# Optimization experiments

Measured on AMD Instinct MI355X. Metric: run time of the kernel, lower is better.

Reference implementation:

```python
import jax, jax.numpy as jnp
import numpy as np

N, F, E = 100000, 128, 600000
EPS = 1e-5

def setup_inputs() -> dict:
    key = jax.random.key(0)
    ks = jax.random.split(key, 12)
    d = {
        'feature': jax.random.normal(ks[0], (N, F), jnp.float32),
        'edge_index': jax.random.randint(ks[1], (2, E), 0, N, jnp.int64 if jax.config.jax_enable_x64 else jnp.int32).astype(jnp.int32),
        'edge_weight': jax.random.uniform(ks[2], (E,), jnp.float32),
        'Ws': jax.random.normal(ks[3], (F, F), jnp.float32) * (2.0 / F) ** 0.5,
        'bs': jnp.zeros((F,), jnp.float32),
        'Wi': jax.random.normal(ks[4], (F, F), jnp.float32) * (2.0 / F) ** 0.5,
        'bi': jnp.zeros((F,), jnp.float32),
        'Wr': jax.random.normal(ks[5], (F, F), jnp.float32) * (2.0 / F) ** 0.5,
        'br': jnp.zeros((F,), jnp.float32),
        'gamma': jnp.ones((F,), jnp.float32),
        'beta': jnp.zeros((F,), jnp.float32),
        'WtoI': jax.random.normal(ks[6], (2 * F, F), jnp.float32) * (1.0 / (2 * F)) ** 0.5,
        'btoI': jnp.zeros((F,), jnp.float32),
        'WtoR': jax.random.normal(ks[7], (F, F), jnp.float32) * (1.0 / F) ** 0.5,
        'btoR': jnp.zeros((F,), jnp.float32),
        'Wout': jax.random.normal(ks[8], (3 * F, 3), jnp.float32) * (2.0 / (3 * F)) ** 0.5,
        'bout': jnp.zeros((3,), jnp.float32),
    }
    return d

def _bn(x, gamma, beta):
    # BatchNorm1d in training mode: batch mean, biased variance
    m = x.mean(axis=0)
    v = x.var(axis=0)
    return gamma * (x - m) * jax.lax.rsqrt(v + EPS) + beta

def reference(feature, edge_index, edge_weight, Ws, bs, Wi, bi, Wr, br,
              gamma, beta, WtoI, btoI, WtoR, btoR, Wout, bout):
    n = feature.shape[0]
    s = jax.nn.relu(_bn(feature @ Ws + bs + feature, gamma, beta))
    i = jax.nn.relu(_bn(feature @ Wi + bi + feature, gamma, beta))
    r = jax.nn.relu(_bn(feature @ Wr + br + feature, gamma, beta))
    # message passing: gather i at source nodes, weight, scatter-add to dest
    src, dst = edge_index[0], edge_index[1]
    msg = i[src] * edge_weight[:, None]                      # [E, F]
    neighbor_i = jax.ops.segment_sum(msg, dst, num_segments=n)  # [N, F]
    toI = jnp.concatenate([s, neighbor_i], axis=1) @ WtoI + btoI
    toR = i @ WtoR + btoR
    s1 = s - toI
    i1 = i + toI - toR
    r1 = toR + r
    logits = jnp.concatenate([s1, i1, r1], axis=-1) @ Wout + bout  # [N, 3]
    return jax.nn.softmax(logits, axis=-1)
```

## Files before the change

kernel.cpp:

```cpp
#include <hip/hip_runtime.h>
#include <math.h>

#define NFEAT 128
#define EPSBN 1e-5f
#define LDA 136
#define NREP 8
#define G1GRID 1536

typedef __attribute__((ext_vector_type(8))) short short8;
typedef __attribute__((ext_vector_type(4))) float f32x4;

__device__ __forceinline__ unsigned short f2bf(float x) {
  union { float f; unsigned u; } v; v.f = x;
  unsigned r = v.u + 0x7FFF + ((v.u >> 16) & 1);
  return (unsigned short)(r >> 16);
}
__device__ __forceinline__ float bf2f(unsigned short h) {
  union { unsigned u; float f; } v; v.u = (unsigned)h << 16;
  return v.f;
}

__global__ __launch_bounds__(256) void kp_params(
    const float* __restrict__ Ws, const float* __restrict__ Wi,
    const float* __restrict__ Wr,
    const float* __restrict__ WtoI, const float* __restrict__ btoI,
    const float* __restrict__ WtoR, const float* __restrict__ btoR,
    const float* __restrict__ Wout, const float* __restrict__ bout,
    short* __restrict__ Whi,
    float* __restrict__ MT, float* __restrict__ cb)
{
  const int tid = threadIdx.x;
  if (blockIdx.x < 24) {
    int t = blockIdx.x * 256 + tid;
    int m   = t >> 11;
    int rem = t & 2047;
    int kf  = rem >> 9;
    int kg  = (rem >> 7) & 3;
    int c   = rem & 127;
    const float* W = (m == 0) ? Ws : ((m == 1) ? Wi : Wr);
    short hb[8];
#pragma unroll
    for (int j = 0; j < 8; j++) {
      int k = kf * 32 + kg * 8 + j;
      float w = W[(size_t)k * NFEAT + c] + (k == c ? 1.0f : 0.0f);
      hb[j] = (short)f2bf(w);
    }
    int base = ((m * 16 + kf * 4 + kg) << 10) + (c << 3);
    *(short8*)&Whi[base] = *(short8*)hb;
    return;
  }

  int t = (blockIdx.x - 24) * 256 + tid;
  int cl = t / 512;
  int idx = t - cl * 512;
  int part = idx >> 7, k = idx & 127;
  float val;
  if (part == 0) {
    float s = Wout[k * 3 + cl];
    for (int f = 0; f < 128; f++)
      s = fmaf(WtoI[k * 128 + f],
               Wout[(128 + f) * 3 + cl] - Wout[f * 3 + cl], s);
    val = s;
  } else if (part == 1) {
    float s = Wout[(128 + k) * 3 + cl];
    for (int f = 0; f < 128; f++)
      s = fmaf(WtoR[k * 128 + f],
               Wout[(256 + f) * 3 + cl] - Wout[(128 + f) * 3 + cl], s);
    val = s;
  } else if (part == 2) {
    val = Wout[(256 + k) * 3 + cl];
  } else {
    float s = 0.f;
    for (int f = 0; f < 128; f++)
      s = fmaf(WtoI[(128 + k) * 128 + f],
               Wout[(128 + f) * 3 + cl] - Wout[f * 3 + cl], s);
    val = s;
  }
  MT[cl * 512 + idx] = val;

  if (blockIdx.x == 24 && tid < 3) {
    float s = bout[tid];
    for (int f = 0; f < 128; f++) {
      s = fmaf(btoI[f], Wout[(128 + f) * 3 + tid] - Wout[f * 3 + tid], s);
      s = fmaf(btoR[f], Wout[(256 + f) * 3 + tid] - Wout[(128 + f) * 3 + tid], s);
    }
    cb[tid] = s;
  }
}

__global__ __launch_bounds__(256) void k1a_store(
    const float* __restrict__ feat,
    const short* __restrict__ Whi,
    const float* __restrict__ bs, const float* __restrict__ bi,
    const float* __restrict__ br,
    float* __restrict__ stats,
    unsigned short* __restrict__ Pb,
    int N, int ntiles)
{
  __shared__ short Ah[32 * LDA];

  const int tid  = threadIdx.x;
  const int lane = tid & 63;
  const int wv   = tid >> 6;
  const int l15  = lane & 15;
  const int kg   = lane >> 4;
  const int krow = kg * 8;
  const int sr   = tid >> 3;
  const int so   = tid & 7;

  const int col0 = wv * 32 + l15;
  const int col1 = wv * 32 + 16 + l15;

  float bias0[3], bias1[3];
  {
    const float* Bm[3] = {bs, bi, br};
#pragma unroll
    for (int m = 0; m < 3; m++) { bias0[m] = Bm[m][col0]; bias1[m] = Bm[m][col1]; }
  }
  float ssum0[3] = {0.f, 0.f, 0.f}, ssq0[3] = {0.f, 0.f, 0.f};
  float ssum1[3] = {0.f, 0.f, 0.f}, ssq1[3] = {0.f, 0.f, 0.f};
  const size_t nf = (size_t)N * NFEAT;

  for (int tile = blockIdx.x; tile < ntiles; tile += gridDim.x) {
    const int row0 = tile * 32;
    {
      int gr = row0 + sr; if (gr >= N) gr = N - 1;
      const float4* s4 = (const float4*)(feat + (size_t)gr * NFEAT + so * 16);
      short hbuf[16];
#pragma unroll
      for (int q = 0; q < 4; q++) {
        float4 f = s4[q];
        float xs[4] = {f.x, f.y, f.z, f.w};
#pragma unroll
        for (int cc = 0; cc < 4; cc++) hbuf[q * 4 + cc] = (short)f2bf(xs[cc]);
      }
      *(short8*)&Ah[sr * LDA + so * 16]     = *(short8*)(hbuf);
      *(short8*)&Ah[sr * LDA + so * 16 + 8] = *(short8*)(hbuf + 8);
    }
    asm volatile("s_waitcnt lgkmcnt(0)" ::: "memory");
    __builtin_amdgcn_s_barrier();

#pragma unroll
    for (int m = 0; m < 3; m++) {
      f32x4 a00 = {0.f,0.f,0.f,0.f}, a01 = {0.f,0.f,0.f,0.f};
      f32x4 a10 = {0.f,0.f,0.f,0.f}, a11 = {0.f,0.f,0.f,0.f};
#pragma unroll
      for (int kf = 0; kf < 4; kf++) {
        int fb0 = ((m * 16 + kf * 4 + kg) << 10) + (col0 << 3);
        int fb1 = ((m * 16 + kf * 4 + kg) << 10) + (col1 << 3);
        short8 b0 = *(const short8*)&Whi[fb0];
        short8 b1 = *(const short8*)&Whi[fb1];
        short8 ar0 = *(const short8*)&Ah[(l15) * LDA + kf * 32 + krow];
        short8 ar1 = *(const short8*)&Ah[(16 + l15) * LDA + kf * 32 + krow];
        a00 = __builtin_amdgcn_mfma_f32_16x16x32_bf16(ar0, b0, a00, 0, 0, 0);
        a01 = __builtin_amdgcn_mfma_f32_16x16x32_bf16(ar1, b0, a01, 0, 0, 0);
        a10 = __builtin_amdgcn_mfma_f32_16x16x32_bf16(ar0, b1, a10, 0, 0, 0);
        a11 = __builtin_amdgcn_mfma_f32_16x16x32_bf16(ar1, b1, a11, 0, 0, 0);
      }
#pragma unroll
      for (int g = 0; g < 4; g++) {
        int gr0 = row0 + kg * 4 + g;
        int gr1 = row0 + 16 + kg * 4 + g;
        if (gr0 < N) {
          float v = a00[g] + bias0[m];
          ssum0[m] += v; ssq0[m] += v * v;
          Pb[(size_t)m * nf + (size_t)gr0 * NFEAT + col0] = f2bf(v);
          float w = a10[g] + bias1[m];
          ssum1[m] += w; ssq1[m] += w * w;
          Pb[(size_t)m * nf + (size_t)gr0 * NFEAT + col1] = f2bf(w);
        }
        if (gr1 < N) {
          float v = a01[g] + bias0[m];
          ssum0[m] += v; ssq0[m] += v * v;
          Pb[(size_t)m * nf + (size_t)gr1 * NFEAT + col0] = f2bf(v);
          float w = a11[g] + bias1[m];
          ssum1[m] += w; ssq1[m] += w * w;
          Pb[(size_t)m * nf + (size_t)gr1 * NFEAT + col1] = f2bf(w);
        }
      }
    }
    asm volatile("s_waitcnt lgkmcnt(0)" ::: "memory");
    __builtin_amdgcn_s_barrier();
  }

#pragma unroll
  for (int m = 0; m < 3; m++) {
    float s0 = ssum0[m], q0 = ssq0[m], s1 = ssum1[m], q1 = ssq1[m];
    s0 += __shfl_xor(s0, 16); s0 += __shfl_xor(s0, 32);
    q0 += __shfl_xor(q0, 16); q0 += __shfl_xor(q0, 32);
    s1 += __shfl_xor(s1, 16); s1 += __shfl_xor(s1, 32);
    q1 += __shfl_xor(q1, 16); q1 += __shfl_xor(q1, 32);
    if (kg == 0) {
      unsafeAtomicAdd(&stats[m * 256 + col0], s0);
      unsafeAtomicAdd(&stats[m * 256 + 128 + col0], q0);
      unsafeAtomicAdd(&stats[m * 256 + col1], s1);
      unsafeAtomicAdd(&stats[m * 256 + 128 + col1], q1);
    }
  }
}

__global__ __launch_bounds__(256) void k1g_post(
    const unsigned short* __restrict__ Pb,
    const float* __restrict__ stats,
    const float* __restrict__ gamma, const float* __restrict__ beta,
    const float* __restrict__ MT,
    float* __restrict__ slogA, float* __restrict__ qv,
    float* __restrict__ logit3R, int N, int N4, int nrt, float invN)
{
  __shared__ float4 A4s[384];
  __shared__ float4 B4s[384];
  const int tid = threadIdx.x;
  for (int i = tid; i < 384; i += 256) {
    int m = i >> 7, c = i & 127;
    float mu = stats[m * 256 + c] * invN;
    float var = stats[m * 256 + 128 + c] * invN - mu * mu;
    float a = gamma[c] * rsqrtf(var + EPSBN);
    float kv = beta[c] - mu * a;
    int idx = m * 128 + (c & 7) * 16 + (c >> 3);
    A4s[idx] = make_float4(MT[0 * 512 + m * 128 + c],
                           MT[1 * 512 + m * 128 + c],
                           MT[2 * 512 + m * 128 + c], a);
    if (m == 1)
      B4s[idx] = make_float4(MT[0 * 512 + 384 + c],
                             MT[1 * 512 + 384 + c],
                             MT[2 * 512 + 384 + c], kv);
    else
      B4s[idx] = make_float4(0.f, 0.f, 0.f, kv);
  }
  __syncthreads();

  const int l15 = tid & 15;
  const int rg  = tid >> 4;
  const size_t nf = (size_t)N * NFEAT;

  for (int it = blockIdx.x; it < nrt; it += gridDim.x) {
    if (tid < 128) {
      int rep = tid >> 4;
      int zr = it * 16 + (tid & 15);
      if (zr < N)
        *(float4*)&logit3R[(size_t)rep * N4 + (size_t)zr * 4] =
            make_float4(0.f, 0.f, 0.f, 0.f);
    }

    int row = it * 16 + rg;
    if (row >= N) continue;

    float s0 = 0.f, s1 = 0.f, s2 = 0.f;
    float q0 = 0.f, q1 = 0.f, q2 = 0.f;
#pragma unroll
    for (int m = 0; m < 3; m++) {
      const uint4* p4 =
          (const uint4*)(Pb + (size_t)m * nf + (size_t)row * NFEAT + l15 * 8);
      uint4 u = p4[0];
      unsigned dw[4] = {u.x, u.y, u.z, u.w};
#pragma unroll
      for (int d = 0; d < 4; d++) {
        {
          float4 ab = A4s[m * 128 + (2 * d) * 16 + l15];
          float4 bq = B4s[m * 128 + (2 * d) * 16 + l15];
          float P = bf2f((unsigned short)(dw[d] & 0xffffu));
          float v = fmaxf(fmaf(ab.w, P, bq.w), 0.f);
          s0 = fmaf(v, ab.x, s0); s1 = fmaf(v, ab.y, s1); s2 = fmaf(v, ab.z, s2);
          q0 = fmaf(v, bq.x, q0); q1 = fmaf(v, bq.y, q1); q2 = fmaf(v, bq.z, q2);
        }
        {
          float4 ab = A4s[m * 128 + (2 * d + 1) * 16 + l15];
          float4 bq = B4s[m * 128 + (2 * d + 1) * 16 + l15];
          float P = bf2f((unsigned short)(dw[d] >> 16));
          float v = fmaxf(fmaf(ab.w, P, bq.w), 0.f);
          s0 = fmaf(v, ab.x, s0); s1 = fmaf(v, ab.y, s1); s2 = fmaf(v, ab.z, s2);
          q0 = fmaf(v, bq.x, q0); q1 = fmaf(v, bq.y, q1); q2 = fmaf(v, bq.z, q2);
        }
      }
    }
#pragma unroll
    for (int off = 1; off < 16; off <<= 1) {
      s0 += __shfl_xor(s0, off); s1 += __shfl_xor(s1, off);
      s2 += __shfl_xor(s2, off);
      q0 += __shfl_xor(q0, off); q1 += __shfl_xor(q1, off);
      q2 += __shfl_xor(q2, off);
    }
    if (l15 == 0) {
      *(float4*)&slogA[(size_t)row * 4] = make_float4(s0, s1, s2, 0.f);
      *(float4*)&qv[(size_t)row * 4]    = make_float4(q0, q1, q2, 0.f);
    }
  }
}

__global__ __launch_bounds__(256) void k_edge(
    const int* __restrict__ eidx, const float* __restrict__ ew,
    const float* __restrict__ q, float* __restrict__ logit3R,
    int E, int N4)
{
  const int wid  = (blockIdx.x * 256 + threadIdx.x) >> 6;
  const int lane = threadIdx.x & 63;
  const int el   = lane / 3;
  const int comp = lane - el * 3;
  if (el >= 21) return;
  const int e = wid * 21 + el;
  if (e >= E) return;

  int src = eidx[e];
  int dst = eidx[E + e];
  float w = ew[e];
  float qvv = q[(size_t)src * 4 + comp];
  int rep = wid & (NREP - 1);
  unsafeAtomicAdd(&logit3R[(size_t)rep * N4 + (size_t)dst * 4 + comp], qvv * w);
}

__global__ __launch_bounds__(256) void k4_final(
    const float* __restrict__ slogA, const float* __restrict__ logit3R,
    const float* __restrict__ cb,
    float* __restrict__ out, int N, int N4)
{
  int r = blockIdx.x * 256 + threadIdx.x;
  if (r >= N) return;
  float4 S = *(const float4*)&slogA[(size_t)r * 4];
  float l0 = S.x + cb[0], l1 = S.y + cb[1], l2 = S.z + cb[2];
#pragma unroll
  for (int rep = 0; rep < NREP; rep++) {
    float4 L = *(const float4*)&logit3R[(size_t)rep * N4 + (size_t)r * 4];
    l0 += L.x; l1 += L.y; l2 += L.z;
  }
  float mx = fmaxf(l0, fmaxf(l1, l2));
  float e0 = expf(l0 - mx), e1 = expf(l1 - mx), e2 = expf(l2 - mx);
  float inv = 1.f / (e0 + e1 + e2);
  out[(size_t)r * 3 + 0] = e0 * inv;
  out[(size_t)r * 3 + 1] = e1 * inv;
  out[(size_t)r * 3 + 2] = e2 * inv;
}

extern "C" void kernel_launch(void* const* d_in, const int* in_sizes, int n_in,
                              void* d_out, int out_size, void* d_ws, size_t ws_size,
                              hipStream_t stream)
{
  const float* feat  = (const float*)d_in[0];
  const int*   eidx  = (const int*)  d_in[1];
  const float* ew    = (const float*)d_in[2];
  const float* Ws    = (const float*)d_in[3];
  const float* bs    = (const float*)d_in[4];
  const float* Wi    = (const float*)d_in[5];
  const float* bi    = (const float*)d_in[6];
  const float* Wr    = (const float*)d_in[7];
  const float* br    = (const float*)d_in[8];
  const float* gamma = (const float*)d_in[9];
  const float* beta  = (const float*)d_in[10];
  const float* WtoI  = (const float*)d_in[11];
  const float* btoI  = (const float*)d_in[12];
  const float* WtoR  = (const float*)d_in[13];
  const float* btoR  = (const float*)d_in[14];
  const float* Wout  = (const float*)d_in[15];
  const float* bout  = (const float*)d_in[16];

  const int N = in_sizes[0] / NFEAT;
  const int E = in_sizes[2];
  const int N4 = 4 * N;
  const float invN = 1.0f / (float)N;
  float* out = (float*)d_out;

  float* logit3R = (float*)d_ws;
  float* slogA   = logit3R + (size_t)NREP * N4;
  float* qv      = slogA + 4 * (size_t)N;
  float* stats   = qv + 4 * (size_t)N;
  float* MT      = stats + 768;
  float* cb      = MT + 1536;
  short* Whi     = (short*)(cb + 4);
  unsigned short* Pb = (unsigned short*)(Whi + 49152);

  hipMemsetAsync(stats, 0, 768 * sizeof(float), stream);

  const int nt32 = (N + 31) / 32;
  const int nrt  = (N + 15) / 16;

  kp_params<<<30, 256, 0, stream>>>(Ws, Wi, Wr, WtoI, btoI, WtoR, btoR,
                                    Wout, bout, Whi, MT, cb);
  k1a_store<<<G1GRID, 256, 0, stream>>>(feat, Whi, bs, bi, br, stats, Pb,
                                        N, nt32);
  k1g_post<<<2048, 256, 0, stream>>>(Pb, stats, gamma, beta, MT,
                                     slogA, qv, logit3R, N, N4, nrt, invN);
  const int nwaves = (E + 20) / 21;
  k_edge<<<(nwaves + 3) / 4, 256, 0, stream>>>(eidx, ew, qv, logit3R, E, N4);
  k4_final<<<(N + 255) / 256, 256, 0, stream>>>(slogA, logit3R, cb, out, N, N4);
}
```

Baseline: 143.1 us.

## Replace BN-stat atomics with per-block partials and dedicated reduction kernel

Each k1a_store block now writes its per-column sum and sum-of-squares into a transposed partials buffer instead of issuing global float atomics into a shared stats array. A new k_redbn kernel reduces the partials per column, computes the BatchNorm scale and shift together with the MT coefficients once, and stores them as float4 tables. k1g_post then just loads these precomputed tables instead of having every block recompute them, and the memset is dropped. The aim is to remove atomic contention and the repeated per-block BN setup, at the cost of an extra kernel launch and roughly 4.7 MB of partials traffic.

Result: faster. 120.8 us (median of 2 runs) (-15.6%).

```diff
diff --git a/kernel.cpp b/kernel.cpp
--- a/kernel.cpp
+++ b/kernel.cpp
@@ -93,7 +93,7 @@
     const short* __restrict__ Whi,
     const float* __restrict__ bs, const float* __restrict__ bi,
     const float* __restrict__ br,
-    float* __restrict__ stats,
+    float* __restrict__ SpartT,
     unsigned short* __restrict__ Pb,
     int N, int ntiles)
 {
@@ -191,42 +191,70 @@
     s1 += __shfl_xor(s1, 16); s1 += __shfl_xor(s1, 32);
     q1 += __shfl_xor(q1, 16); q1 += __shfl_xor(q1, 32);
     if (kg == 0) {
-      unsafeAtomicAdd(&stats[m * 256 + col0], s0);
-      unsafeAtomicAdd(&stats[m * 256 + 128 + col0], q0);
-      unsafeAtomicAdd(&stats[m * 256 + col1], s1);
-      unsafeAtomicAdd(&stats[m * 256 + 128 + col1], q1);
-    }
+      SpartT[(size_t)(m * 256 + col0) * G1GRID + blockIdx.x]       = s0;
+      SpartT[(size_t)(m * 256 + 128 + col0) * G1GRID + blockIdx.x] = q0;
+      SpartT[(size_t)(m * 256 + col1) * G1GRID + blockIdx.x]       = s1;
+      SpartT[(size_t)(m * 256 + 128 + col1) * G1GRID + blockIdx.x] = q1;
+    }
+  }
+}
+
+__global__ __launch_bounds__(256) void k_redbn(
+    const float* __restrict__ SpartT,
+    const float* __restrict__ gamma, const float* __restrict__ beta,
+    const float* __restrict__ MT,
+    float4* __restrict__ A4, float4* __restrict__ B4, float invN)
+{
+  __shared__ float reds[8];
+  const int tid = threadIdx.x;
+  const int j = blockIdx.x;
+  const int m = j >> 7, c = j & 127;
+  const size_t rowS = (size_t)(m * 256 + c) * G1GRID;
+  const size_t rowQ = (size_t)(m * 256 + 128 + c) * G1GRID;
+
+  float s = 0.f, q = 0.f;
+#pragma unroll
+  for (int k = 0; k < G1GRID / 256; k++) {
+    s += SpartT[rowS + k * 256 + tid];
+    q += SpartT[rowQ + k * 256 + tid];
+  }
+#pragma unroll
+  for (int off = 1; off < 64; off <<= 1) {
+    s += __shfl_xor(s, off);
+    q += __shfl_xor(q, off);
+  }
+  if ((tid & 63) == 0) { reds[tid >> 6] = s; reds[4 + (tid >> 6)] = q; }
+  __syncthreads();
+  if (tid == 0) {
+    float sum = (reds[0] + reds[1]) + (reds[2] + reds[3]);
+    float ssq = (reds[4] + reds[5]) + (reds[6] + reds[7]);
+    float mu = sum * invN;
+    float var = ssq * invN - mu * mu;
+    float a = gamma[c] * rsqrtf(var + EPSBN);
+    float kv = beta[c] - mu * a;
+    int idx = m * 128 + (c & 7) * 16 + (c >> 3);
+    A4[idx] = make_float4(MT[0 * 512 + m * 128 + c],
+                          MT[1 * 512 + m * 128 + c],
+                          MT[2 * 512 + m * 128 + c], a);
+    if (m == 1)
+      B4[idx] = make_float4(MT[0 * 512 + 384 + c],
+                            MT[1 * 512 + 384 + c],
+                            MT[2 * 512 + 384 + c], kv);
+    else
+      B4[idx] = make_float4(0.f, 0.f, 0.f, kv);
   }
 }
 
 __global__ __launch_bounds__(256) void k1g_post(
     const unsigned short* __restrict__ Pb,
-    const float* __restrict__ stats,
-    const float* __restrict__ gamma, const float* __restrict__ beta,
-    const float* __restrict__ MT,
+    const float4* __restrict__ A4, const float4* __restrict__ B4,
     float* __restrict__ slogA, float* __restrict__ qv,
-    float* __restrict__ logit3R, int N, int N4, int nrt, float invN)
+    float* __restrict__ logit3R, int N, int N4, int nrt)
 {
   __shared__ float4 A4s[384];
   __shared__ float4 B4s[384];
   const int tid = threadIdx.x;
-  for (int i = tid; i < 384; i += 256) {
-    int m = i >> 7, c = i & 127;
-    float mu = stats[m * 256 + c] * invN;
-    float var = stats[m * 256 + 128 + c] * invN - mu * mu;
-    float a = gamma[c] * rsqrtf(var + EPSBN);
-    float kv = beta[c] - mu * a;
-    int idx = m * 128 + (c & 7) * 16 + (c >> 3);
-    A4s[idx] = make_float4(MT[0 * 512 + m * 128 + c],
-                           MT[1 * 512 + m * 128 + c],
-                           MT[2 * 512 + m * 128 + c], a);
-    if (m == 1)
-      B4s[idx] = make_float4(MT[0 * 512 + 384 + c],
-                             MT[1 * 512 + 384 + c],
-                             MT[2 * 512 + 384 + c], kv);
-    else
-      B4s[idx] = make_float4(0.f, 0.f, 0.f, kv);
-  }
+  for (int i = tid; i < 384; i += 256) { A4s[i] = A4[i]; B4s[i] = B4[i]; }
   __syncthreads();
 
   const int l15 = tid & 15;
@@ -361,23 +389,24 @@
   float* logit3R = (float*)d_ws;
   float* slogA   = logit3R + (size_t)NREP * N4;
   float* qv      = slogA + 4 * (size_t)N;
-  float* stats   = qv + 4 * (size_t)N;
-  float* MT      = stats + 768;
+  float* MT      = qv + 4 * (size_t)N;
   float* cb      = MT + 1536;
-  short* Whi     = (short*)(cb + 4);
+  float4* A4     = (float4*)(cb + 4 + 12);
+  float4* B4     = A4 + 384;
+  float* SpartT  = (float*)(B4 + 384);
+  short* Whi     = (short*)(SpartT + (size_t)768 * G1GRID);
   unsigned short* Pb = (unsigned short*)(Whi + 49152);
-
-  hipMemsetAsync(stats, 0, 768 * sizeof(float), stream);
 
   const int nt32 = (N + 31) / 32;
   const int nrt  = (N + 15) / 16;
 
   kp_params<<<30, 256, 0, stream>>>(Ws, Wi, Wr, WtoI, btoI, WtoR, btoR,
                                     Wout, bout, Whi, MT, cb);
-  k1a_store<<<G1GRID, 256, 0, stream>>>(feat, Whi, bs, bi, br, stats, Pb,
+  k1a_store<<<G1GRID, 256, 0, stream>>>(feat, Whi, bs, bi, br, SpartT, Pb,
                                         N, nt32);
-  k1g_post<<<2048, 256, 0, stream>>>(Pb, stats, gamma, beta, MT,
-                                     slogA, qv, logit3R, N, N4, nrt, invN);
+  k_redbn<<<384, 256, 0, stream>>>(SpartT, gamma, beta, MT, A4, B4, invN);
+  k1g_post<<<2048, 256, 0, stream>>>(Pb, A4, B4, slogA, qv, logit3R,
+                                     N, N4, nrt);
   const int nwaves = (E + 20) / 21;
   k_edge<<<(nwaves + 3) / 4, 256, 0, stream>>>(eidx, ew, qv, logit3R, E, N4);
   k4_final<<<(N + 255) / 256, 256, 0, stream>>>(slogA, logit3R, cb, out, N, N4);
```
